# Performance work log

Measured on AMD Instinct MI355X. Metric: run time of the kernel, lower is better.

Reference implementation:

```python
import jax, jax.numpy as jnp
import numpy as np

# hp / hp_mask constants
B = 1024          # batch_size
S = 4096          # seq_length (raw timesteps)
PATCH = 8         # patch_size
P = S // PATCH    # num patches = 512 (second dim of x)
K = 128           # dimension
P_M, P_R, P_E = 0.8, 0.1, 0.1
CORR = 0.15       # Corruption_ratio
NUM_MASK = int(B * P_M)
NUM_RAND = int(B * P_R)
MAX_CORR = int(CORR * S / PATCH)  # max corrupted patches per row = 76


def setup_inputs() -> dict:
    key = jax.random.key(0)
    k1, k2, k3, k4 = jax.random.split(key, 4)
    x = jax.random.normal(k1, (B, P, K), dtype=jnp.float32)
    pos = jax.random.normal(k2, (P, K), dtype=jnp.float32)
    w_mask = jax.random.normal(k3, (K,), dtype=jnp.float32)  # nn.Linear(1,K,bias=False) weight col
    seq_len = jax.random.randint(k4, (B,), PATCH, S + 1)     # per-sample raw length
    return {"x": x, "pos": pos, "w_mask": w_mask, "seq_len": seq_len}


def reference(x, pos, w_mask, seq_len):
    key = jax.random.key(42)
    kp, ks, kr = jax.random.split(key, 3)

    # --- batch-level mask_type assignment (permute batch, split into 3 groups) ---
    perm = jax.random.permutation(kp, B)
    mask_type = jnp.zeros((B,), dtype=jnp.float32)
    mask_type = mask_type.at[perm[:NUM_MASK]].set(0.0)
    mask_type = mask_type.at[perm[NUM_MASK:NUM_MASK + NUM_RAND]].set(1.0)
    mask_type = mask_type.at[perm[NUM_MASK + NUM_RAND:]].set(2.0)

    # --- per-row sampling without replacement over valid patches ---
    n_valid = (seq_len // PATCH).astype(jnp.int32)                                   # [B]
    n_corr = jnp.floor(CORR * seq_len.astype(jnp.float32) / PATCH).astype(jnp.int32)  # [B]
    scores = jax.random.uniform(ks, (B, P))
    valid = jnp.arange(P)[None, :] < n_valid[:, None]
    scores = jnp.where(valid, scores, jnp.inf)
    order = jnp.argsort(scores, axis=1)   # [B,P] patch ids, random order among valid first
    rank = jnp.argsort(order, axis=1)     # rank of each patch position
    sel = rank < n_corr[:, None]          # [B,P] bool: patch selected for corruption

    # padded index output (replaces ragged list I; -1 = pad)
    slot_valid = jnp.arange(MAX_CORR)[None, :] < n_corr[:, None]
    I = jnp.where(slot_valid, order[:, :MAX_CORR], -1)

    # --- replacement values (branch on mask_type[0], as in the original code) ---
    mask_vec = w_mask                                        # Linear(1,K)(1.0)
    rand_vals = jax.random.uniform(kr, (B, P, K))
    repl_mask = mask_vec[None, None, :] + pos[None, :, :]    # [1,P,K] -> broadcast
    repl_rand = rand_vals + pos[None, :, :]                  # [B,P,K]
    t0 = mask_type[0]
    repl = jnp.where(t0 == 0.0, repl_mask, jnp.where(t0 == 1.0, repl_rand, x))
    x_out = jnp.where(sel[:, :, None], repl, x)
    return x_out, I, mask_type
```

## Files before the change

### kernel.cpp

```cpp
#include <hip/hip_runtime.h>
#include <cstdint>
#include <cstring>

#define JAX_PARTITIONABLE 1

#define B_ 1024
#define P_ 512
#define K_ 128
#define MAXC 76
#define NSCORE 524288ull
#define NRAND  67108864ull
#define OFF_I  ((size_t)B_ * P_ * K_)
#define OFF_MT (OFF_I + (size_t)B_ * MAXC)

typedef float f4 __attribute__((ext_vector_type(4)));

struct MTPack { uint32_t w[B_ / 16]; };

__host__ __device__ inline uint32_t rotl32(uint32_t v, int d) {
    return (v << d) | (v >> (32 - d));
}

__host__ __device__ inline void tf2x32(uint32_t k0, uint32_t k1,
                                       uint32_t x0, uint32_t x1,
                                       uint32_t& o0, uint32_t& o1) {
    uint32_t ks2 = k0 ^ k1 ^ 0x1BD11BDAu;
    x0 += k0; x1 += k1;
#define TF_R(r) { x0 += x1; x1 = rotl32(x1, (r)); x1 ^= x0; }
    TF_R(13) TF_R(15) TF_R(26) TF_R(6)
    x0 += k1;  x1 += ks2 + 1u;
    TF_R(17) TF_R(29) TF_R(16) TF_R(24)
    x0 += ks2; x1 += k0 + 2u;
    TF_R(13) TF_R(15) TF_R(26) TF_R(6)
    x0 += k0;  x1 += k1 + 3u;
    TF_R(17) TF_R(29) TF_R(16) TF_R(24)
    x0 += k1;  x1 += ks2 + 4u;
    TF_R(13) TF_R(15) TF_R(26) TF_R(6)
    x0 += ks2; x1 += k0 + 5u;
#undef TF_R
    o0 = x0; o1 = x1;
}

__host__ __device__ inline uint32_t jax_bits(uint32_t k0, uint32_t k1,
                                             uint64_t i, uint64_t n) {
#if JAX_PARTITIONABLE
    (void)n;
    uint32_t o0, o1;
    tf2x32(k0, k1, (uint32_t)(i >> 32), (uint32_t)i, o0, o1);
    return o0 ^ o1;
#else
    uint64_t half = n >> 1;
    uint32_t o0, o1;
    if (i < half) { tf2x32(k0, k1, (uint32_t)i, (uint32_t)(i + half), o0, o1); return o0; }
    tf2x32(k0, k1, (uint32_t)(i - half), (uint32_t)i, o0, o1); return o1;
#endif
}

__device__ inline float u01(uint32_t bits) {
    return __uint_as_float((bits >> 9) | 0x3F800000u) - 1.0f;
}

template <int T0>
__global__ void __launch_bounds__(256) fused_kernel(const float* __restrict__ x,
                                                    const float* __restrict__ pos,
                                                    const float* __restrict__ wm,
                                                    const int* __restrict__ seq_len,
                                                    float* __restrict__ out,
                                                    float* __restrict__ I_out,
                                                    float* __restrict__ mt_out,
                                                    MTPack mtp,
                                                    uint32_t ks0, uint32_t ks1,
                                                    uint32_t kr0, uint32_t kr1) {
    int b = blockIdx.x;
    int tid = threadIdx.x;
    __shared__ float sc[P_];
    __shared__ uint32_t selmask[P_ / 32];

    int sl = seq_len[b];
    int n_valid = sl >> 3;
    int n_corr = (int)floorf(0.15f * (float)sl / 8.0f);

    if (tid < P_ / 32) selmask[tid] = 0u;

    if (b == 0) {
        for (int j = tid; j < B_; j += 256)
            mt_out[j] = (float)((mtp.w[j >> 4] >> ((j & 15) * 2)) & 3u);
    }

    if (tid < MAXC && tid >= n_corr) I_out[(size_t)b * MAXC + tid] = -1.0f;

    if (n_corr > 0) {
        for (int p = tid; p < P_; p += 256) {
            float s = __builtin_inff();
            if (p < n_valid) {
                uint32_t bits = jax_bits(ks0, ks1, (uint64_t)b * P_ + p, NSCORE);
                s = u01(bits);
            }
            sc[p] = s;
        }
        __syncthreads();

        int p0 = tid, p1 = tid + 256;
        bool a0 = p0 < n_valid;
        bool a1 = p1 < n_valid;
        if (a0 | a1) {
            float s0 = sc[p0];
            float s1 = sc[p1];
            int r0 = 0, r1 = 0;
            for (int q = 0; q < n_valid; q++) {
                float sq = sc[q];
                r0 += (sq < s0) || (sq == s0 && q < p0);
                r1 += (sq < s1) || (sq == s1 && q < p1);
            }
            if (a0 && r0 < n_corr) {
                I_out[(size_t)b * MAXC + r0] = (float)p0;
                atomicOr(&selmask[p0 >> 5], 1u << (p0 & 31));
            }
            if (a1 && r1 < n_corr) {
                I_out[(size_t)b * MAXC + r1] = (float)p1;
                atomicOr(&selmask[p1 >> 5], 1u << (p1 & 31));
            }
        }
    }
    __syncthreads();

    const f4* x4  = (const f4*)x + (size_t)b * (P_ * (K_ / 4));
    f4*       o4  = (f4*)out     + (size_t)b * (P_ * (K_ / 4));
    const f4* p4  = (const f4*)pos;
    const f4* wm4 = (const f4*)wm;

    for (int i = tid; i < P_ * (K_ / 4); i += 256) {
        f4 v;
        if (T0 == 2) {
            v = __builtin_nontemporal_load(&x4[i]);
        } else {
            int p  = i >> 5;
            bool sel = (selmask[p >> 5] >> (p & 31)) & 1u;
            if (!sel) {
                v = __builtin_nontemporal_load(&x4[i]);
            } else {
                int kq = i & 31;
                f4 c = p4[p * (K_ / 4) + kq];
                if (T0 == 0) {
                    v = wm4[kq] + c;
                } else {
                    uint64_t e = (((uint64_t)b * P_ + p) * K_) + (uint64_t)kq * 4;
                    v.x = u01(jax_bits(kr0, kr1, e + 0, NRAND)) + c.x;
                    v.y = u01(jax_bits(kr0, kr1, e + 1, NRAND)) + c.y;
                    v.z = u01(jax_bits(kr0, kr1, e + 2, NRAND)) + c.z;
                    v.w = u01(jax_bits(kr0, kr1, e + 3, NRAND)) + c.w;
                }
            }
        }
        __builtin_nontemporal_store(v, &o4[i]);
    }
}

extern "C" void kernel_launch(void* const* d_in, const int* in_sizes, int n_in,
                              void* d_out, int out_size, void* d_ws, size_t ws_size,
                              hipStream_t stream) {
    (void)in_sizes; (void)n_in; (void)d_ws; (void)ws_size; (void)out_size;
    const float* x   = (const float*)d_in[0];
    const float* pos = (const float*)d_in[1];
    const float* wm  = (const float*)d_in[2];
    const int* seq_len = (const int*)d_in[3];
    float* out = (float*)d_out;

    static bool init_done = false;
    static MTPack mtp;
    static int t0 = 0;
    static uint32_t ks0, ks1, kr0, kr1;
    if (!init_done) {
        uint32_t kp0, kp1, sub0, sub1;
#if JAX_PARTITIONABLE
        tf2x32(0u, 42u, 0u, 0u, kp0, kp1);
        tf2x32(0u, 42u, 0u, 1u, ks0, ks1);
        tf2x32(0u, 42u, 0u, 2u, kr0, kr1);
        tf2x32(kp0, kp1, 0u, 1u, sub0, sub1);
#else
        {
            uint32_t a0, b0, a1, b1, a2, b2;
            tf2x32(0u, 42u, 0u, 3u, a0, b0);
            tf2x32(0u, 42u, 1u, 4u, a1, b1);
            tf2x32(0u, 42u, 2u, 5u, a2, b2);
            kp0 = a0; kp1 = a1; ks0 = a2; ks1 = b0; kr0 = b1; kr1 = b2;
            uint32_t c0, d0, c1, d1;
            tf2x32(kp0, kp1, 0u, 2u, c0, d0);
            tf2x32(kp0, kp1, 1u, 3u, c1, d1);
            sub0 = d0; sub1 = d1;
        }
#endif
        static uint32_t skeys[B_];
        for (int i = 0; i < B_; i++)
            skeys[i] = jax_bits(sub0, sub1, (uint64_t)i, (uint64_t)B_);
        memset(&mtp, 0, sizeof(mtp));
        for (int i = 0; i < B_; i++) {
            uint32_t ki = skeys[i];
            int rank = 0;
            for (int q = 0; q < B_; q++) {
                uint32_t kq = skeys[q];
                rank += (kq < ki) || (kq == ki && q < i);
            }
            uint32_t code = rank < 819 ? 0u : (rank < 921 ? 1u : 2u);
            mtp.w[i >> 4] |= code << ((i & 15) * 2);
        }
        t0 = (int)(mtp.w[0] & 3u);
        init_done = true;
    }

    float* I_out  = out + OFF_I;
    float* mt_out = out + OFF_MT;

    switch (t0) {
    case 0:
        fused_kernel<0><<<dim3(B_), dim3(256), 0, stream>>>(
            x, pos, wm, seq_len, out, I_out, mt_out, mtp, ks0, ks1, kr0, kr1);
        break;
    case 1:
        fused_kernel<1><<<dim3(B_), dim3(256), 0, stream>>>(
            x, pos, wm, seq_len, out, I_out, mt_out, mtp, ks0, ks1, kr0, kr1);
        break;
    default:
        fused_kernel<2><<<dim3(B_), dim3(256), 0, stream>>>(
            x, pos, wm, seq_len, out, I_out, mt_out, mtp, ks0, ks1, kr0, kr1);
        break;
    }
}
```

Measured before the change: 451.3 us.

## Use 512-thread blocks, one patch per thread for ranking, batched copy loads

After: 443.0 us. Within noise of the previous version (-1.8%).

```diff
diff --git a/kernel.cpp b/kernel.cpp
--- a/kernel.cpp
+++ b/kernel.cpp
@@ -61,16 +61,17 @@
 }
 
 template <int T0>
-__global__ void __launch_bounds__(256) fused_kernel(const float* __restrict__ x,
-                                                    const float* __restrict__ pos,
-                                                    const float* __restrict__ wm,
-                                                    const int* __restrict__ seq_len,
-                                                    float* __restrict__ out,
-                                                    float* __restrict__ I_out,
-                                                    float* __restrict__ mt_out,
-                                                    MTPack mtp,
-                                                    uint32_t ks0, uint32_t ks1,
-                                                    uint32_t kr0, uint32_t kr1) {
+__global__ void __launch_bounds__(512, (T0 == 1 ? 4 : 8))
+fused_kernel(const float* __restrict__ x,
+             const float* __restrict__ pos,
+             const float* __restrict__ wm,
+             const int* __restrict__ seq_len,
+             float* __restrict__ out,
+             float* __restrict__ I_out,
+             float* __restrict__ mt_out,
+             MTPack mtp,
+             uint32_t ks0, uint32_t ks1,
+             uint32_t kr0, uint32_t kr1) {
     int b = blockIdx.x;
     int tid = threadIdx.x;
     __shared__ float sc[P_];
@@ -83,42 +84,39 @@
     if (tid < P_ / 32) selmask[tid] = 0u;
 
     if (b == 0) {
-        for (int j = tid; j < B_; j += 256)
+        for (int j = tid; j < B_; j += 512)
             mt_out[j] = (float)((mtp.w[j >> 4] >> ((j & 15) * 2)) & 3u);
     }
 
     if (tid < MAXC && tid >= n_corr) I_out[(size_t)b * MAXC + tid] = -1.0f;
 
     if (n_corr > 0) {
-        for (int p = tid; p < P_; p += 256) {
+        {
             float s = __builtin_inff();
-            if (p < n_valid) {
-                uint32_t bits = jax_bits(ks0, ks1, (uint64_t)b * P_ + p, NSCORE);
+            if (tid < n_valid) {
+                uint32_t bits = jax_bits(ks0, ks1, (uint64_t)b * P_ + tid, NSCORE);
                 s = u01(bits);
             }
-            sc[p] = s;
+            sc[tid] = s;
         }
         __syncthreads();
 
-        int p0 = tid, p1 = tid + 256;
-        bool a0 = p0 < n_valid;
-        bool a1 = p1 < n_valid;
-        if (a0 | a1) {
-            float s0 = sc[p0];
-            float s1 = sc[p1];
-            int r0 = 0, r1 = 0;
-            for (int q = 0; q < n_valid; q++) {
-                float sq = sc[q];
-                r0 += (sq < s0) || (sq == s0 && q < p0);
-                r1 += (sq < s1) || (sq == s1 && q < p1);
-            }
-            if (a0 && r0 < n_corr) {
-                I_out[(size_t)b * MAXC + r0] = (float)p0;
-                atomicOr(&selmask[p0 >> 5], 1u << (p0 & 31));
-            }
-            if (a1 && r1 < n_corr) {
-                I_out[(size_t)b * MAXC + r1] = (float)p1;
-                atomicOr(&selmask[p1 >> 5], 1u << (p1 & 31));
+        if (tid < n_valid) {
+            float sp = sc[tid];
+            int rank = 0;
+            const f4* sc4 = (const f4*)sc;
+            int nq4 = (n_valid + 3) >> 2;
+            for (int q4 = 0; q4 < nq4; q4++) {
+                f4 s4 = sc4[q4];
+                int qb = q4 << 2;
+                rank += (s4.x < sp) || (s4.x == sp && qb + 0 < tid);
+                rank += (s4.y < sp) || (s4.y == sp && qb + 1 < tid);
+                rank += (s4.z < sp) || (s4.z == sp && qb + 2 < tid);
+                rank += (s4.w < sp) || (s4.w == sp && qb + 3 < tid);
+            }
+            if (rank < n_corr) {
+                I_out[(size_t)b * MAXC + rank] = (float)tid;
+                atomicOr(&selmask[tid >> 5], 1u << (tid & 31));
             }
         }
     }
@@ -129,30 +127,47 @@
     const f4* p4  = (const f4*)pos;
     const f4* wm4 = (const f4*)wm;
 
-    for (int i = tid; i < P_ * (K_ / 4); i += 256) {
-        f4 v;
-        if (T0 == 2) {
-            v = __builtin_nontemporal_load(&x4[i]);
-        } else {
-            int p  = i >> 5;
-            bool sel = (selmask[p >> 5] >> (p & 31)) & 1u;
-            if (!sel) {
-                v = __builtin_nontemporal_load(&x4[i]);
-            } else {
-                int kq = i & 31;
-                f4 c = p4[p * (K_ / 4) + kq];
-                if (T0 == 0) {
-                    v = wm4[kq] + c;
-                } else {
-                    uint64_t e = (((uint64_t)b * P_ + p) * K_) + (uint64_t)kq * 4;
-                    v.x = u01(jax_bits(kr0, kr1, e + 0, NRAND)) + c.x;
-                    v.y = u01(jax_bits(kr0, kr1, e + 1, NRAND)) + c.y;
-                    v.z = u01(jax_bits(kr0, kr1, e + 2, NRAND)) + c.z;
-                    v.w = u01(jax_bits(kr0, kr1, e + 3, NRAND)) + c.w;
+    if (T0 == 2) {
+        for (int k = 0; k < 32; k += 4) {
+            f4 v[4];
+#pragma unroll
+            for (int u = 0; u < 4; u++)
+                v[u] = __builtin_nontemporal_load(&x4[tid + (k + u) * 512]);
+#pragma unroll
+            for (int u = 0; u < 4; u++)
+                __builtin_nontemporal_store(v[u], &o4[tid + (k + u) * 512]);
+        }
+    } else {
+        const int kq = tid & 31;
+        const int pb = tid >> 5;
+        f4 wmv;
+        if (T0 == 0) wmv = wm4[kq];
+        for (int k = 0; k < 32; k += 4) {
+            f4 v[4];
+#pragma unroll
+            for (int u = 0; u < 4; u++)
+                v[u] = __builtin_nontemporal_load(&x4[tid + (k + u) * 512]);
+#pragma unroll
+            for (int u = 0; u < 4; u++) {
+                int pp = pb + (k + u) * 16;
+                bool sel = (selmask[pp >> 5] >> (pp & 31)) & 1u;
+                if (sel) {
+                    f4 c = p4[pp * (K_ / 4) + kq];
+                    if (T0 == 0) {
+                        v[u] = wmv + c;
+                    } else {
+                        uint64_t e = (((uint64_t)b * P_ + pp) * K_) + (uint64_t)kq * 4;
+                        v[u].x = u01(jax_bits(kr0, kr1, e + 0, NRAND)) + c.x;
+                        v[u].y = u01(jax_bits(kr0, kr1, e + 1, NRAND)) + c.y;
+                        v[u].z = u01(jax_bits(kr0, kr1, e + 2, NRAND)) + c.z;
+                        v[u].w = u01(jax_bits(kr0, kr1, e + 3, NRAND)) + c.w;
+                    }
                 }
             }
-        }
-        __builtin_nontemporal_store(v, &o4[i]);
+#pragma unroll
+            for (int u = 0; u < 4; u++)
+                __builtin_nontemporal_store(v[u], &o4[tid + (k + u) * 512]);
+        }
     }
 }
 
@@ -213,15 +228,15 @@
 
     switch (t0) {
     case 0:
-        fused_kernel<0><<<dim3(B_), dim3(256), 0, stream>>>(
+        fused_kernel<0><<<dim3(B_), dim3(512), 0, stream>>>(
             x, pos, wm, seq_len, out, I_out, mt_out, mtp, ks0, ks1, kr0, kr1);
         break;
     case 1:
-        fused_kernel<1><<<dim3(B_), dim3(256), 0, stream>>>(
+        fused_kernel<1><<<dim3(B_), dim3(512), 0, stream>>>(
             x, pos, wm, seq_len, out, I_out, mt_out, mtp, ks0, ks1, kr0, kr1);
         break;
     default:
-        fused_kernel<2><<<dim3(B_), dim3(256), 0, stream>>>(
+        fused_kernel<2><<<dim3(B_), dim3(512), 0, stream>>>(
             x, pos, wm, seq_len, out, I_out, mt_out, mtp, ks0, ks1, kr0, kr1);
         break;
     }
```
